# Performance work log

Measured on AMD Instinct MI355X. Metric: run time of the kernel, lower is better.

Reference implementation:

```python
import jax, jax.numpy as jnp
import numpy as np

BOX_W, CLS_W, OBJ_W = 0.05, 0.5, 1.0


def setup_inputs() -> dict:
    key = jax.random.key(0)
    k1, k2, k3 = jax.random.split(key, 3)
    predictions = jax.random.normal(k1, (16, 3, 160, 160, 9), dtype=jnp.float32)
    coords = jax.random.uniform(k2, (16, 32, 4), dtype=jnp.float32)  # xy, wh in [0,1)
    cls = jax.random.randint(k3, (16, 32, 1), 0, 4).astype(jnp.float32)
    targets = jnp.concatenate([cls, coords], axis=-1)  # [B, T, 5]: class, x, y, w, h
    return {"predictions": predictions, "targets": targets}


def _loss(predictions, targets):
    B = predictions.shape[0]
    D = predictions.shape[-1]
    T = targets.shape[1]

    def per_image(pred, tgt):
        pred = pred.reshape(-1, D)                 # [P, D]
        pxy, pwh = pred[:, :2], pred[:, 2:4]
        pobj, pcls = pred[:, 4], pred[:, 5:]
        txy, twh = tgt[:, 1:3], tgt[:, 3:5]
        tcls = tgt[:, 0].astype(jnp.int32)
        # pairwise IoU [P, T]
        p1, p2 = pxy - pwh / 2, pxy + pwh / 2
        t1, t2 = txy - twh / 2, txy + twh / 2
        lo = jnp.maximum(p1[:, None, :], t1[None, :, :])
        hi = jnp.minimum(p2[:, None, :], t2[None, :, :])
        inter = jnp.prod(jnp.clip(hi - lo, 0.0), axis=-1)
        pa = jnp.prod(p2 - p1, axis=-1)[:, None]
        ta = jnp.prod(t2 - t1, axis=-1)[None, :]
        iou = (inter / (pa + ta - inter + 1e-6)).max(axis=1)   # [P]
        pos = iou > 0.5
        neg = iou < 0.3
        posf = pos.astype(pred.dtype)
        negf = neg.astype(pred.dtype)
        npos = posf.sum()
        nneg = negf.sum()
        # k-th positive prediction pairs with target[k mod T] (torch .repeat semantics)
        rank = jnp.cumsum(pos.astype(jnp.int32)) - 1
        tidx = jnp.maximum(rank, 0) % T
        # box: MSE over positive pred_xy vs tiled target_xy (mean over elems)
        sq = (pxy - txy[tidx]) ** 2                # [P, 2]
        box = jnp.where(npos > 0, (sq * posf[:, None]).sum() / (2.0 * npos), 0.0)
        # cls: cross entropy over positives
        logp = jax.nn.log_softmax(pcls, axis=-1)
        ce = -jnp.take_along_axis(logp, tcls[tidx][:, None], axis=-1)[:, 0]
        cls = jnp.where(npos > 0, (ce * posf).sum() / npos, 0.0)
        # obj: BCE-with-logits, target 1 on positives, 0 on negatives
        obj = jnp.where(npos > 0, (jax.nn.softplus(-pobj) * posf).sum() / npos, 0.0) \
            + jnp.where(nneg > 0, (jax.nn.softplus(pobj) * negf).sum() / nneg, 0.0)
        return box, cls, obj

    box, cls, obj = jax.vmap(per_image)(predictions, targets)
    box_loss = box.sum() / B
    cls_loss = cls.sum() / B
    obj_loss = obj.sum() / B
    total = BOX_W * box_loss + CLS_W * cls_loss + OBJ_W * obj_loss
    return total, box_loss, cls_loss, obj_loss


def reference(predictions, targets):
    return _loss(predictions, targets)
```

## Files before the change

kernel.cpp:

```cpp
#include <hip/hip_runtime.h>
#include <cstdint>
#include <cstddef>

constexpr int kB     = 16;
constexpr int kN     = 76800;
constexpr int kD     = 9;
constexpr int kT     = 32;
constexpr int kBlk1  = 256;
constexpr int kNB1   = kN / kBlk1;
constexpr int kBlk3  = 512;
constexpr int kNB3   = kN / kBlk3;
constexpr int kWords = kN / 64;

struct ImgStats { int npos; int nneg; float objPos; float objNeg; };

__device__ __forceinline__ float softplusf(float x) {
  return fmaxf(x, 0.f) + log1pf(expf(-fabsf(x)));
}

__global__ __launch_bounds__(kB * kT) void pass0_kernel(
    const float* __restrict__ tgt, float* __restrict__ twork)
{
  const int t = threadIdx.x;
  const int b = t >> 5, j = t & 31;
  const float* tp = tgt + ((size_t)b * kT + j) * 5;
  const float tx = tp[1], ty = tp[2], tw = tp[3], th = tp[4];
  const float t1x = tx - tw * 0.5f, t1y = ty - th * 0.5f;
  const float t2x = tx + tw * 0.5f, t2y = ty + th * 0.5f;
  float* w = twork + (size_t)b * 5 * kT;
  w[0 * kT + j] = t1x;
  w[1 * kT + j] = t1y;
  w[2 * kT + j] = t2x;
  w[3 * kT + j] = t2y;
  w[4 * kT + j] = (t2x - t1x) * (t2y - t1y);
}

__global__ __launch_bounds__(kBlk1) void pass1_kernel(
    const float* __restrict__ pred, const float* __restrict__ twork,
    int* __restrict__ blockCounts, int* __restrict__ blockNneg,
    float* __restrict__ blockObjP, float* __restrict__ blockObjN,
    unsigned long long* __restrict__ posBits)
{
  __shared__ float s_red[4][2];
  __shared__ int   s_cnt[4][2];

  const int b   = blockIdx.y;
  const int blk = blockIdx.x;
  const int tid = threadIdx.x;
  const float* tw = twork + (size_t)b * 5 * kT;

  const int i = blk * kBlk1 + tid;
  const float* p = pred + ((size_t)b * kN + i) * kD;
  const float px = p[0], py = p[1], pw = p[2], ph = p[3], pobj = p[4];
  const float p1x = px - pw * 0.5f, p1y = py - ph * 0.5f;
  const float p2x = px + pw * 0.5f, p2y = py + ph * 0.5f;
  const float pa  = (p2x - p1x) * (p2y - p1y);

  bool posAny = false, negAll = true;
  #pragma unroll
  for (int j = 0; j < kT; ++j) {
    const float t1x = tw[0 * kT + j];
    const float t1y = tw[1 * kT + j];
    const float t2x = tw[2 * kT + j];
    const float t2y = tw[3 * kT + j];
    const float ta  = tw[4 * kT + j];
    const float lox = fmaxf(p1x, t1x), loy = fmaxf(p1y, t1y);
    const float hix = fminf(p2x, t2x), hiy = fminf(p2y, t2y);
    const float inter = fmaxf(hix - lox, 0.f) * fmaxf(hiy - loy, 0.f);
    const float d = ((pa + ta) - inter) + 1e-6f;
    posAny = posAny || ((d >= 0.f) && (inter > 0.5f * d));
    negAll = negAll && ((d <  0.f) || (inter < 0.3f * d));
  }
  const bool pos = posAny;
  const bool neg = negAll;

  const float op = pos ? softplusf(-pobj) : 0.f;
  const float on = neg ? softplusf( pobj) : 0.f;

  const int lane = tid & 63;
  const int wv   = tid >> 6;
  const unsigned long long pmask = __ballot(pos);
  const unsigned long long nmask = __ballot(neg);
  if (lane == 0)
    posBits[(size_t)b * kWords + blk * 4 + wv] = pmask;

  float rop = op, ron = on;
  #pragma unroll
  for (int off = 32; off > 0; off >>= 1) {
    rop += __shfl_down(rop, off, 64);
    ron += __shfl_down(ron, off, 64);
  }
  if (lane == 0) {
    s_red[wv][0] = rop;              s_red[wv][1] = ron;
    s_cnt[wv][0] = __popcll(pmask);  s_cnt[wv][1] = __popcll(nmask);
  }
  __syncthreads();
  if (tid == 0) {
    float sop = 0.f, son = 0.f; int pc = 0, nc = 0;
    #pragma unroll
    for (int w = 0; w < 4; ++w) {
      sop += s_red[w][0]; son += s_red[w][1];
      pc  += s_cnt[w][0]; nc  += s_cnt[w][1];
    }
    const int slot = b * kNB1 + blk;
    blockCounts[slot] = pc;
    blockNneg[slot]   = nc;
    blockObjP[slot]   = sop;
    blockObjN[slot]   = son;
  }
}

__global__ __launch_bounds__(512) void pass2_kernel(
    const int* __restrict__ blockCounts, const int* __restrict__ blockNneg,
    const float* __restrict__ blockObjP, const float* __restrict__ blockObjN,
    int* __restrict__ blockOffsets, ImgStats* __restrict__ stats)
{
  __shared__ int s[512];
  __shared__ float s_op[8], s_on[8];
  __shared__ int   s_nn[8];

  const int b = blockIdx.x, t = threadIdx.x;
  const bool live = (t < kNB1);
  const int v = live ? blockCounts[b * kNB1 + t] : 0;
  int   nn = live ? blockNneg[b * kNB1 + t] : 0;
  float op = live ? blockObjP[b * kNB1 + t] : 0.f;
  float on = live ? blockObjN[b * kNB1 + t] : 0.f;

  s[t] = v;
  __syncthreads();
  for (int off = 1; off < 512; off <<= 1) {
    const int add = (t >= off) ? s[t - off] : 0;
    __syncthreads();
    s[t] += add;
    __syncthreads();
  }
  if (live) blockOffsets[b * kNB1 + t] = s[t] - v;

  const int lane = t & 63, wv = t >> 6;
  #pragma unroll
  for (int off = 32; off > 0; off >>= 1) {
    nn += __shfl_down(nn, off, 64);
    op += __shfl_down(op, off, 64);
    on += __shfl_down(on, off, 64);
  }
  if (lane == 0) { s_nn[wv] = nn; s_op[wv] = op; s_on[wv] = on; }
  __syncthreads();
  if (t == 0) {
    int tn = 0; float top = 0.f, ton = 0.f;
    #pragma unroll
    for (int w = 0; w < 8; ++w) { tn += s_nn[w]; top += s_op[w]; ton += s_on[w]; }
    ImgStats st;
    st.npos = s[511];
    st.nneg = tn;
    st.objPos = top;
    st.objNeg = ton;
    stats[b] = st;
  }
}

__global__ __launch_bounds__(kBlk3) void pass3_kernel(
    const float* __restrict__ pred, const float* __restrict__ tgt,
    const int* __restrict__ blockOffsets,
    const unsigned long long* __restrict__ posBits,
    float* __restrict__ p3sq, float* __restrict__ p3ce)
{
  __shared__ float s_tx[kT], s_ty[kT];
  __shared__ int   s_tc[kT];
  __shared__ int   s_wtot[8];
  __shared__ float s_red[8][2];

  const int b = blockIdx.y, blk = blockIdx.x, tid = threadIdx.x;
  const int slot = b * kNB3 + blk;
  const int lane = tid & 63, wv = tid >> 6;
  const unsigned long long mask = posBits[(size_t)b * kWords + blk * 8 + wv];
  if (lane == 0) s_wtot[wv] = __popcll(mask);
  __syncthreads();

  int tot = 0;
  #pragma unroll
  for (int w = 0; w < 8; ++w) tot += s_wtot[w];
  if (tot == 0) {
    if (tid == 0) { p3sq[slot] = 0.f; p3ce[slot] = 0.f; }
    return;
  }

  if (tid < kT) {
    const float* tp = tgt + ((size_t)b * kT + tid) * 5;
    s_tx[tid] = tp[1]; s_ty[tid] = tp[2];
    s_tc[tid] = (int)tp[0];
  }
  __syncthreads();

  int base = blockOffsets[b * kNB1 + blk * 2];
  for (int w = 0; w < wv; ++w) base += s_wtot[w];

  const bool pos = (mask >> lane) & 1ull;
  float sqc = 0.f, cec = 0.f;
  if (pos) {
    const int ord = base + __popcll(mask & ((1ull << lane) - 1ull));
    const int tix = ord & (kT - 1);
    const int i = blk * kBlk3 + tid;
    const float* p = pred + ((size_t)b * kN + i) * kD;
    const float dx = p[0] - s_tx[tix];
    const float dy = p[1] - s_ty[tix];
    sqc = dx * dx + dy * dy;
    const float c0 = p[5], c1 = p[6], c2 = p[7], c3 = p[8];
    const float m = fmaxf(fmaxf(c0, c1), fmaxf(c2, c3));
    const float lse = m + logf(expf(c0 - m) + expf(c1 - m) + expf(c2 - m) + expf(c3 - m));
    const int tc = s_tc[tix];
    const float cv = (tc == 0) ? c0 : (tc == 1) ? c1 : (tc == 2) ? c2 : c3;
    cec = lse - cv;
  }
  #pragma unroll
  for (int off = 32; off > 0; off >>= 1) {
    sqc += __shfl_down(sqc, off, 64);
    cec += __shfl_down(cec, off, 64);
  }
  if (lane == 0) { s_red[wv][0] = sqc; s_red[wv][1] = cec; }
  __syncthreads();
  if (tid == 0) {
    float ss = 0.f, cs = 0.f;
    #pragma unroll
    for (int w = 0; w < 8; ++w) { ss += s_red[w][0]; cs += s_red[w][1]; }
    p3sq[slot] = ss;
    p3ce[slot] = cs;
  }
}

__global__ __launch_bounds__(256) void pass4_kernel(
    const ImgStats* __restrict__ stats,
    const float* __restrict__ p3sq, const float* __restrict__ p3ce,
    float* __restrict__ out)
{
  __shared__ float s_sq[16][17], s_ce[16][17];
  const int tid = threadIdx.x;
  const int b = tid & 15, g = tid >> 4;
  float sq = 0.f, ce = 0.f;
  for (int k = g; k < kNB3; k += 16) {
    sq += p3sq[b * kNB3 + k];
    ce += p3ce[b * kNB3 + k];
  }
  s_sq[g][b] = sq; s_ce[g][b] = ce;
  __syncthreads();

  float box = 0.f, cls = 0.f, obj = 0.f;
  if (tid < kB) {
    float ssq = 0.f, sce = 0.f;
    #pragma unroll
    for (int gg = 0; gg < 16; ++gg) { ssq += s_sq[gg][tid]; sce += s_ce[gg][tid]; }
    const ImgStats st = stats[tid];
    const float np_ = (float)st.npos;
    const float nn  = (float)st.nneg;
    if (np_ > 0.f) {
      box = ssq / (2.0f * np_);
      cls = sce / np_;
      obj = st.objPos / np_;
    }
    if (nn > 0.f) obj += st.objNeg / nn;
  }
  #pragma unroll
  for (int off = 8; off > 0; off >>= 1) {
    box += __shfl_down(box, off, 64);
    cls += __shfl_down(cls, off, 64);
    obj += __shfl_down(obj, off, 64);
  }
  if (tid == 0) {
    box *= (1.f / 16.f); cls *= (1.f / 16.f); obj *= (1.f / 16.f);
    out[0] = 0.05f * box + 0.5f * cls + 1.0f * obj;
    out[1] = box;
    out[2] = cls;
    out[3] = obj;
  }
}

extern "C" void kernel_launch(void* const* d_in, const int* in_sizes, int n_in,
                              void* d_out, int out_size, void* d_ws, size_t ws_size,
                              hipStream_t stream)
{
  const float* pred = (const float*)d_in[0];
  const float* tgt  = (const float*)d_in[1];
  float* out = (float*)d_out;

  char* ws = (char*)d_ws;
  float* twork        = (float*)(ws);
  int*   blockCounts  = (int*)(ws + 10240);
  int*   blockNneg    = (int*)(ws + 29440);
  float* blockObjP    = (float*)(ws + 48640);
  float* blockObjN    = (float*)(ws + 67840);
  int*   blockOffsets = (int*)(ws + 87040);
  ImgStats* stats     = (ImgStats*)(ws + 106240);
  unsigned long long* posBits =
      (unsigned long long*)(ws + 106496);
  float* p3sq         = (float*)(ws + 260096);
  float* p3ce         = (float*)(ws + 269696);

  pass0_kernel<<<1, kB * kT, 0, stream>>>(tgt, twork);
  pass1_kernel<<<dim3(kNB1, kB), kBlk1, 0, stream>>>(
      pred, twork, blockCounts, blockNneg, blockObjP, blockObjN, posBits);
  pass2_kernel<<<dim3(kB), 512, 0, stream>>>(
      blockCounts, blockNneg, blockObjP, blockObjN, blockOffsets, stats);
  pass3_kernel<<<dim3(kNB3, kB), kBlk3, 0, stream>>>(
      pred, tgt, blockOffsets, posBits, p3sq, p3ce);
  pass4_kernel<<<1, 256, 0, stream>>>(stats, p3sq, p3ce, out);
}
```

Baseline: 117.8 us.

## Process four anchors per thread with vectorized float4 loads in IoU pass

```diff
diff --git a/kernel.cpp b/kernel.cpp
--- a/kernel.cpp
+++ b/kernel.cpp
@@ -7,9 +7,8 @@
 constexpr int kD     = 9;
 constexpr int kT     = 32;
 constexpr int kBlk1  = 256;
-constexpr int kNB1   = kN / kBlk1;
-constexpr int kBlk3  = 512;
-constexpr int kNB3   = kN / kBlk3;
+constexpr int kApB   = 1024;
+constexpr int kNB    = kN / kApB;
 constexpr int kWords = kN / 64;
 
 struct ImgStats { int npos; int nneg; float objPos; float objNeg; };
@@ -35,28 +34,44 @@
   w[4 * kT + j] = (t2x - t1x) * (t2y - t1y);
 }
 
-__global__ __launch_bounds__(kBlk1) void pass1_kernel(
+__global__ __launch_bounds__(kBlk1) void k1_iou_kernel(
     const float* __restrict__ pred, const float* __restrict__ twork,
-    int* __restrict__ blockCounts, int* __restrict__ blockNneg,
-    float* __restrict__ blockObjP, float* __restrict__ blockObjN,
+    int* __restrict__ cnt, int* __restrict__ nnegA,
+    float* __restrict__ objP, float* __restrict__ objN,
     unsigned long long* __restrict__ posBits)
 {
   __shared__ float s_red[4][2];
   __shared__ int   s_cnt[4][2];
 
-  const int b   = blockIdx.y;
-  const int blk = blockIdx.x;
-  const int tid = threadIdx.x;
+  const int b    = blockIdx.y;
+  const int blk  = blockIdx.x;
+  const int tid  = threadIdx.x;
+  const int lane = tid & 63;
+  const int wv   = tid >> 6;
   const float* tw = twork + (size_t)b * 5 * kT;
 
-  const int i = blk * kBlk1 + tid;
-  const float* p = pred + ((size_t)b * kN + i) * kD;
-  const float px = p[0], py = p[1], pw = p[2], ph = p[3], pobj = p[4];
-  const float p1x = px - pw * 0.5f, p1y = py - ph * 0.5f;
-  const float p2x = px + pw * 0.5f, p2y = py + ph * 0.5f;
-  const float pa  = (p2x - p1x) * (p2y - p1y);
-
-  bool posAny = false, negAll = true;
+  const int a0 = blk * kApB + wv * 256 + 4 * lane;
+  const float4* q = reinterpret_cast<const float4*>(
+      pred + ((size_t)b * kN + a0) * kD);
+  const float4 q0 = q[0], q1 = q[1], q2 = q[2], q3 = q[3];
+  const float4 q4 = q[4], q5 = q[5], q6 = q[6], q7 = q[7];
+
+  float px[4], py[4], pw_[4], ph[4], pobj[4];
+  px[0]=q0.x; py[0]=q0.y; pw_[0]=q0.z; ph[0]=q0.w; pobj[0]=q1.x;
+  px[1]=q2.y; py[1]=q2.z; pw_[1]=q2.w; ph[1]=q3.x; pobj[1]=q3.y;
+  px[2]=q4.z; py[2]=q4.w; pw_[2]=q5.x; ph[2]=q5.y; pobj[2]=q5.z;
+  px[3]=q6.w; py[3]=q7.x; pw_[3]=q7.y; ph[3]=q7.z; pobj[3]=q7.w;
+
+  float p1x[4], p1y[4], p2x[4], p2y[4], pa[4];
+  #pragma unroll
+  for (int k = 0; k < 4; ++k) {
+    p1x[k] = px[k] - pw_[k] * 0.5f;  p1y[k] = py[k] - ph[k] * 0.5f;
+    p2x[k] = px[k] + pw_[k] * 0.5f;  p2y[k] = py[k] + ph[k] * 0.5f;
+    pa[k]  = (p2x[k] - p1x[k]) * (p2y[k] - p1y[k]);
+  }
+
+  bool posA[4] = {false,false,false,false};
+  bool negA[4] = {true,true,true,true};
   #pragma unroll
   for (int j = 0; j < kT; ++j) {
     const float t1x = tw[0 * kT + j];
@@ -64,55 +79,60 @@
     const float t2x = tw[2 * kT + j];
     const float t2y = tw[3 * kT + j];
     const float ta  = tw[4 * kT + j];
-    const float lox = fmaxf(p1x, t1x), loy = fmaxf(p1y, t1y);
-    const float hix = fminf(p2x, t2x), hiy = fminf(p2y, t2y);
-    const float inter = fmaxf(hix - lox, 0.f) * fmaxf(hiy - loy, 0.f);
-    const float d = ((pa + ta) - inter) + 1e-6f;
-    posAny = posAny || ((d >= 0.f) && (inter > 0.5f * d));
-    negAll = negAll && ((d <  0.f) || (inter < 0.3f * d));
-  }
-  const bool pos = posAny;
-  const bool neg = negAll;
-
-  const float op = pos ? softplusf(-pobj) : 0.f;
-  const float on = neg ? softplusf( pobj) : 0.f;
-
-  const int lane = tid & 63;
-  const int wv   = tid >> 6;
-  const unsigned long long pmask = __ballot(pos);
-  const unsigned long long nmask = __ballot(neg);
-  if (lane == 0)
-    posBits[(size_t)b * kWords + blk * 4 + wv] = pmask;
-
-  float rop = op, ron = on;
+    #pragma unroll
+    for (int k = 0; k < 4; ++k) {
+      const float lox = fmaxf(p1x[k], t1x), loy = fmaxf(p1y[k], t1y);
+      const float hix = fminf(p2x[k], t2x), hiy = fminf(p2y[k], t2y);
+      const float inter = fmaxf(hix - lox, 0.f) * fmaxf(hiy - loy, 0.f);
+      const float d = ((pa[k] + ta) - inter) + 1e-6f;
+      posA[k] = posA[k] || ((d >= 0.f) && (inter > 0.5f * d));
+      negA[k] = negA[k] && ((d <  0.f) || (inter < 0.3f * d));
+    }
+  }
+
+  float op = 0.f, on = 0.f;
+  int pc = 0, nc = 0;
+  const int chunk = blk * 4 + wv;
+  #pragma unroll
+  for (int k = 0; k < 4; ++k) {
+    op += posA[k] ? softplusf(-pobj[k]) : 0.f;
+    on += negA[k] ? softplusf( pobj[k]) : 0.f;
+    const unsigned long long pm = __ballot(posA[k]);
+    const unsigned long long nm = __ballot(negA[k]);
+    if (lane == 0)
+      posBits[(size_t)b * kWords + chunk * 4 + k] = pm;
+    pc += __popcll(pm);
+    nc += __popcll(nm);
+  }
+
   #pragma unroll
   for (int off = 32; off > 0; off >>= 1) {
-    rop += __shfl_down(rop, off, 64);
-    ron += __shfl_down(ron, off, 64);
+    op += __shfl_down(op, off, 64);
+    on += __shfl_down(on, off, 64);
   }
   if (lane == 0) {
-    s_red[wv][0] = rop;              s_red[wv][1] = ron;
-    s_cnt[wv][0] = __popcll(pmask);  s_cnt[wv][1] = __popcll(nmask);
+    s_red[wv][0] = op;  s_red[wv][1] = on;
+    s_cnt[wv][0] = pc;  s_cnt[wv][1] = nc;
   }
   __syncthreads();
   if (tid == 0) {
-    float sop = 0.f, son = 0.f; int pc = 0, nc = 0;
+    float sop = 0.f, son = 0.f; int tpc = 0, tnc = 0;
     #pragma unroll
     for (int w = 0; w < 4; ++w) {
       sop += s_red[w][0]; son += s_red[w][1];
-      pc  += s_cnt[w][0]; nc  += s_cnt[w][1];
+      tpc += s_cnt[w][0]; tnc += s_cnt[w][1];
     }
-    const int slot = b * kNB1 + blk;
-    blockCounts[slot] = pc;
-    blockNneg[slot]   = nc;
-    blockObjP[slot]   = sop;
-    blockObjN[slot]   = son;
+    const int slot = b * kNB + blk;
+    cnt[slot]   = tpc;
+    nnegA[slot] = tnc;
+    objP[slot]  = sop;
+    objN[slot]  = son;
   }
 }
 
 __global__ __launch_bounds__(512) void pass2_kernel(
-    const int* __restrict__ blockCounts, const int* __restrict__ blockNneg,
-    const float* __restrict__ blockObjP, const float* __restrict__ blockObjN,
+    const int* __restrict__ cnt, const int* __restrict__ nnegA,
+    const float* __restrict__ objP, const float* __restrict__ objN,
     int* __restrict__ blockOffsets, ImgStats* __restrict__ stats)
 {
   __shared__ int s[512];
@@ -120,11 +140,11 @@
   __shared__ int   s_nn[8];
 
   const int b = blockIdx.x, t = threadIdx.x;
-  const bool live = (t < kNB1);
-  const int v = live ? blockCounts[b * kNB1 + t] : 0;
-  int   nn = live ? blockNneg[b * kNB1 + t] : 0;
-  float op = live ? blockObjP[b * kNB1 + t] : 0.f;
-  float on = live ? blockObjN[b * kNB1 + t] : 0.f;
+  const bool live = (t < kNB);
+  const int v = live ? cnt[b * kNB + t] : 0;
+  int   nn = live ? nnegA[b * kNB + t] : 0;
+  float op = live ? objP[b * kNB + t] : 0.f;
+  float on = live ? objN[b * kNB + t] : 0.f;
 
   s[t] = v;
   __syncthreads();
@@ -134,7 +154,7 @@
     s[t] += add;
     __syncthreads();
   }
-  if (live) blockOffsets[b * kNB1 + t] = s[t] - v;
+  if (live) blockOffsets[b * kNB + t] = s[t] - v;
 
   const int lane = t & 63, wv = t >> 6;
   #pragma unroll
@@ -158,7 +178,7 @@
   }
 }
 
-__global__ __launch_bounds__(kBlk3) void pass3_kernel(
+__global__ __launch_bounds__(kBlk1) void k2_pos_kernel(
     const float* __restrict__ pred, const float* __restrict__ tgt,
     const int* __restrict__ blockOffsets,
     const unsigned long long* __restrict__ posBits,
@@ -166,23 +186,18 @@
 {
   __shared__ float s_tx[kT], s_ty[kT];
   __shared__ int   s_tc[kT];
-  __shared__ int   s_wtot[8];
-  __shared__ float s_red[8][2];
+  __shared__ int   s_ctot[4];
+  __shared__ float s_red[4][2];
 
   const int b = blockIdx.y, blk = blockIdx.x, tid = threadIdx.x;
-  const int slot = b * kNB3 + blk;
+  const int slot = b * kNB + blk;
   const int lane = tid & 63, wv = tid >> 6;
-  const unsigned long long mask = posBits[(size_t)b * kWords + blk * 8 + wv];
-  if (lane == 0) s_wtot[wv] = __popcll(mask);
-  __syncthreads();
-
-  int tot = 0;
-  #pragma unroll
-  for (int w = 0; w < 8; ++w) tot += s_wtot[w];
-  if (tot == 0) {
-    if (tid == 0) { p3sq[slot] = 0.f; p3ce[slot] = 0.f; }
-    return;
-  }
+
+  const unsigned long long* wp =
+      posBits + (size_t)b * kWords + (blk * 4 + wv) * 4;
+  const unsigned long long m0 = wp[0], m1 = wp[1], m2 = wp[2], m3 = wp[3];
+  const int ctot = __popcll(m0) + __popcll(m1) + __popcll(m2) + __popcll(m3);
+  if (lane == 0) s_ctot[wv] = ctot;
 
   if (tid < kT) {
     const float* tp = tgt + ((size_t)b * kT + tid) * 5;
@@ -191,26 +206,48 @@
   }
   __syncthreads();
 
-  int base = blockOffsets[b * kNB1 + blk * 2];
-  for (int w = 0; w < wv; ++w) base += s_wtot[w];
-
-  const bool pos = (mask >> lane) & 1ull;
+  int tot = 0;
+  #pragma unroll
+  for (int c = 0; c < 4; ++c) tot += s_ctot[c];
+  if (tot == 0) {
+    if (tid == 0) { p3sq[slot] = 0.f; p3ce[slot] = 0.f; }
+    return;
+  }
+
+  int base = blockOffsets[b * kNB + blk];
+  for (int c = 0; c < wv; ++c) base += s_ctot[c];
+
+  const unsigned long long low = ((unsigned long long)1 << lane) - 1ull;
+  const int beforeLanes = __popcll(m0 & low) + __popcll(m1 & low)
+                        + __popcll(m2 & low) + __popcll(m3 & low);
+  const int bit0 = (int)((m0 >> lane) & 1ull);
+  const int bit1 = (int)((m1 >> lane) & 1ull);
+  const int bit2 = (int)((m2 >> lane) & 1ull);
+  const int bit3 = (int)((m3 >> lane) & 1ull);
+  const int kbit[4] = {bit0, bit1, bit2, bit3};
+
+  const int a0 = blk * kApB + wv * 256 + 4 * lane;
   float sqc = 0.f, cec = 0.f;
-  if (pos) {
-    const int ord = base + __popcll(mask & ((1ull << lane) - 1ull));
-    const int tix = ord & (kT - 1);
-    const int i = blk * kBlk3 + tid;
-    const float* p = pred + ((size_t)b * kN + i) * kD;
-    const float dx = p[0] - s_tx[tix];
-    const float dy = p[1] - s_ty[tix];
-    sqc = dx * dx + dy * dy;
-    const float c0 = p[5], c1 = p[6], c2 = p[7], c3 = p[8];
-    const float m = fmaxf(fmaxf(c0, c1), fmaxf(c2, c3));
-    const float lse = m + logf(expf(c0 - m) + expf(c1 - m) + expf(c2 - m) + expf(c3 - m));
-    const int tc = s_tc[tix];
-    const float cv = (tc == 0) ? c0 : (tc == 1) ? c1 : (tc == 2) ? c2 : c3;
-    cec = lse - cv;
-  }
+  int prior = 0;
+  #pragma unroll
+  for (int k = 0; k < 4; ++k) {
+    if (kbit[k]) {
+      const int ord = base + beforeLanes + prior;
+      const int tix = ord & (kT - 1);
+      const float* p = pred + ((size_t)b * kN + (a0 + k)) * kD;
+      const float dx = p[0] - s_tx[tix];
+      const float dy = p[1] - s_ty[tix];
+      sqc += dx * dx + dy * dy;
+      const float c0 = p[5], c1 = p[6], c2 = p[7], c3 = p[8];
+      const float m = fmaxf(fmaxf(c0, c1), fmaxf(c2, c3));
+      const float lse = m + logf(expf(c0 - m) + expf(c1 - m) + expf(c2 - m) + expf(c3 - m));
+      const int tc = s_tc[tix];
+      const float cv = (tc == 0) ? c0 : (tc == 1) ? c1 : (tc == 2) ? c2 : c3;
+      cec += lse - cv;
+    }
+    prior += kbit[k];
+  }
+
   #pragma unroll
   for (int off = 32; off > 0; off >>= 1) {
     sqc += __shfl_down(sqc, off, 64);
@@ -221,7 +258,7 @@
   if (tid == 0) {
     float ss = 0.f, cs = 0.f;
     #pragma unroll
-    for (int w = 0; w < 8; ++w) { ss += s_red[w][0]; cs += s_red[w][1]; }
+    for (int w = 0; w < 4; ++w) { ss += s_red[w][0]; cs += s_red[w][1]; }
     p3sq[slot] = ss;
     p3ce[slot] = cs;
   }
@@ -236,9 +273,9 @@
   const int tid = threadIdx.x;
   const int b = tid & 15, g = tid >> 4;
   float sq = 0.f, ce = 0.f;
-  for (int k = g; k < kNB3; k += 16) {
-    sq += p3sq[b * kNB3 + k];
-    ce += p3ce[b * kNB3 + k];
+  for (int k = g; k < kNB; k += 16) {
+    sq += p3sq[b * kNB + k];
+    ce += p3ce[b * kNB + k];
   }
   s_sq[g][b] = sq; s_ce[g][b] = ce;
   __syncthreads();
@@ -283,23 +320,23 @@
 
   char* ws = (char*)d_ws;
   float* twork        = (float*)(ws);
-  int*   blockCounts  = (int*)(ws + 10240);
-  int*   blockNneg    = (int*)(ws + 29440);
-  float* blockObjP    = (float*)(ws + 48640);
-  float* blockObjN    = (float*)(ws + 67840);
-  int*   blockOffsets = (int*)(ws + 87040);
-  ImgStats* stats     = (ImgStats*)(ws + 106240);
+  int*   cnt          = (int*)(ws + 10240);
+  int*   nnegA        = (int*)(ws + 15104);
+  float* objP         = (float*)(ws + 19968);
+  float* objN         = (float*)(ws + 24832);
+  int*   blockOffsets = (int*)(ws + 29696);
+  ImgStats* stats     = (ImgStats*)(ws + 34560);
   unsigned long long* posBits =
-      (unsigned long long*)(ws + 106496);
-  float* p3sq         = (float*)(ws + 260096);
-  float* p3ce         = (float*)(ws + 269696);
+      (unsigned long long*)(ws + 34816);
+  float* p3sq         = (float*)(ws + 188416);
+  float* p3ce         = (float*)(ws + 193280);
 
   pass0_kernel<<<1, kB * kT, 0, stream>>>(tgt, twork);
-  pass1_kernel<<<dim3(kNB1, kB), kBlk1, 0, stream>>>(
-      pred, twork, blockCounts, blockNneg, blockObjP, blockObjN, posBits);
+  k1_iou_kernel<<<dim3(kNB, kB), kBlk1, 0, stream>>>(
+      pred, twork, cnt, nnegA, objP, objN, posBits);
   pass2_kernel<<<dim3(kB), 512, 0, stream>>>(
-      blockCounts, blockNneg, blockObjP, blockObjN, blockOffsets, stats);
-  pass3_kernel<<<dim3(kNB3, kB), kBlk3, 0, stream>>>(
+      cnt, nnegA, objP, objN, blockOffsets, stats);
+  k2_pos_kernel<<<dim3(kNB, kB), kBlk1, 0, stream>>>(
       pred, tgt, blockOffsets, posBits, p3sq, p3ce);
   pass4_kernel<<<1, 256, 0, stream>>>(stats, p3sq, p3ce, out);
 }
```

Result: no change. 119.9 us (+1.7%).
